# Performance work log

Hardware: AMD Instinct MI355X
Metric: run time of the kernel (lower is better)

Reference implementation:

```python
import jax, jax.numpy as jnp
import numpy as np

NUM_HEADS = 8
D_MODEL = 512
D_Q = D_MODEL // NUM_HEADS
B, S = 4, 2048


def setup_inputs() -> dict:
    key = jax.random.key(0)
    ks = jax.random.split(key, 7)
    bound = 1.0 / np.sqrt(D_MODEL)  # kaiming_uniform with a=sqrt(5) on fan_in=d_model
    return {
        "x_query": jax.random.normal(ks[0], (B, S, D_MODEL), dtype=jnp.float32),
        "x_key": jax.random.normal(ks[1], (B, S, D_MODEL), dtype=jnp.float32),
        "x_value": jax.random.normal(ks[2], (B, S, D_MODEL), dtype=jnp.float32),
        "Q": jax.random.uniform(ks[3], (NUM_HEADS, D_MODEL, D_Q), minval=-bound, maxval=bound, dtype=jnp.float32),
        "K": jax.random.uniform(ks[4], (NUM_HEADS, D_MODEL, D_Q), minval=-bound, maxval=bound, dtype=jnp.float32),
        "V": jax.random.uniform(ks[5], (NUM_HEADS, D_MODEL, D_Q), minval=-bound, maxval=bound, dtype=jnp.float32),
        "Wout": jax.random.uniform(ks[6], (D_MODEL, D_MODEL), minval=-bound, maxval=bound, dtype=jnp.float32),
    }


def reference(x_query, x_key, x_value, Q, K, V, Wout):
    # per-head projections: [B,S,d_model] x [H,d_model,d_q] -> [B,H,S,d_q]
    q = jnp.einsum('bsd,hdq->bhsq', x_query, Q)
    k = jnp.einsum('bsd,hdq->bhsq', x_key, K)
    v = jnp.einsum('bsd,hdq->bhsq', x_value, V)
    scale = 1.0 / jnp.sqrt(jnp.asarray(q.shape[-1], q.dtype))
    scores = jnp.einsum('bhsq,bhtq->bhst', q, k) * scale  # [B,H,S,S]
    attn = jax.nn.softmax(scores, axis=-1)
    heads = jnp.einsum('bhst,bhtq->bhsq', attn, v)  # [B,H,S,d_q]
    # faithful to original: .view(B, S, -1) on [B,H,S,d_q] layout (no transpose)
    concat = heads.reshape(heads.shape[0], heads.shape[2], -1)
    return concat @ Wout.T
```

## Files before the change

kernel.cpp:

```cpp
#include <hip/hip_runtime.h>
#include <math.h>

#define BATCH 4
#define SEQ   2048
#define DM    512
#define NH    8
#define DQ    64
#define BS    (BATCH*SEQ)
#define APAD  72

#define QSCALE 0.18033688011112042f

typedef short  short8   __attribute__((ext_vector_type(8)));
typedef float  floatx4  __attribute__((ext_vector_type(4)));
typedef float  floatx16 __attribute__((ext_vector_type(16)));
typedef unsigned short ushort8 __attribute__((ext_vector_type(8)));
typedef unsigned uintx2 __attribute__((ext_vector_type(2)));
typedef unsigned uintx4 __attribute__((ext_vector_type(4)));

__device__ __forceinline__ unsigned short f2bf(float f) {
    return (unsigned short)((__float_as_uint(f) + 0x8000u) >> 16);
}
__device__ __forceinline__ unsigned pack2bf(float a, float b) {
    unsigned ua = __float_as_uint(a) + 0x8000u;
    unsigned ub = __float_as_uint(b) + 0x8000u;
    return __builtin_amdgcn_perm(ub, ua, 0x07060302u);
}

__global__ __launch_bounds__(256) void convert_w_kernel(
    const float* __restrict__ Wq, const float* __restrict__ Wk,
    const float* __restrict__ Wv, const float* __restrict__ Wo,
    unsigned short* __restrict__ wt, unsigned short* __restrict__ wo)
{
    const int which = blockIdx.y;
    const int idx = blockIdx.x * 256 + threadIdx.x;
    if (which == 3) {
        float4 v = *(const float4*)(Wo + (size_t)idx * 4);
        uint2 o;
        o.x = pack2bf(v.x, v.y);
        o.y = pack2bf(v.z, v.w);
        *(uint2*)(wo + (size_t)idx * 4) = o;
    } else {
        const float* W = (which == 0) ? Wq : (which == 1) ? Wk : Wv;
        const int n   = idx >> 7;
        const int dd0 = (idx & 127) * 4;
        const int h = n >> 6, d = n & 63;
        uint2 o;
        o.x = pack2bf(W[((size_t)h * DM + dd0 + 0) * DQ + d],
                      W[((size_t)h * DM + dd0 + 1) * DQ + d]);
        o.y = pack2bf(W[((size_t)h * DM + dd0 + 2) * DQ + d],
                      W[((size_t)h * DM + dd0 + 3) * DQ + d]);
        *(uint2*)(wt + (size_t)which * (DM * DM) + (size_t)n * DM + dd0) = o;
    }
}

__global__ __launch_bounds__(256) void qkv_gemm_kernel(
    const float* __restrict__ Xq, const float* __restrict__ Xk,
    const float* __restrict__ Xv, const unsigned short* __restrict__ wt,
    unsigned short* __restrict__ Oq, unsigned short* __restrict__ Ok,
    unsigned short* __restrict__ Ovt)
{
    __shared__ unsigned short As[128][APAD];
    __shared__ unsigned short Bs[128][APAD];

    const int which = blockIdx.z;
    const float* X = (which == 0) ? Xq : (which == 1) ? Xk : Xv;
    const unsigned short* Bt = wt + (size_t)which * (DM * DM);

    const int m0 = blockIdx.x * 128;
    const int n0 = blockIdx.y * 128;
    const int t = threadIdx.x, w = t >> 6, lane = t & 63;
    const int quad = lane >> 4, qr = lane & 15;
    const int arow = t >> 4;
    const int acol = (t & 15) * 4;
    const int brow = t >> 3;
    const int bcol = (t & 7) * 8;
    const int mw = 64 * (w >> 1), nw = 64 * (w & 1);

    floatx4 acc[4][4] = {};
    float4  areg[8];
    ushort8 breg[4];

    #pragma unroll
    for (int i = 0; i < 8; ++i)
        areg[i] = *(const float4*)(X + (size_t)(m0 + i * 16 + arow) * DM + acol);
    #pragma unroll
    for (int i = 0; i < 4; ++i)
        breg[i] = *(const ushort8*)(Bt + (size_t)(n0 + i * 32 + brow) * DM + bcol);

    for (int k0 = 0; k0 < DM; k0 += 64) {
        __syncthreads();
        #pragma unroll
        for (int i = 0; i < 8; ++i) {
            uint2 o;
            o.x = pack2bf(areg[i].x, areg[i].y);
            o.y = pack2bf(areg[i].z, areg[i].w);
            *(uint2*)&As[i * 16 + arow][acol] = o;
        }
        #pragma unroll
        for (int i = 0; i < 4; ++i)
            *(ushort8*)&Bs[i * 32 + brow][bcol] = breg[i];
        __syncthreads();

        if (k0 + 64 < DM) {
            #pragma unroll
            for (int i = 0; i < 8; ++i)
                areg[i] = *(const float4*)(X + (size_t)(m0 + i * 16 + arow) * DM + k0 + 64 + acol);
            #pragma unroll
            for (int i = 0; i < 4; ++i)
                breg[i] = *(const ushort8*)(Bt + (size_t)(n0 + i * 32 + brow) * DM + k0 + 64 + bcol);
        }

        #pragma unroll
        for (int kh = 0; kh < 2; ++kh) {
            short8 af[4], bf[4];
            #pragma unroll
            for (int si = 0; si < 4; ++si)
                af[si] = *(const short8*)&As[mw + 16 * si + qr][kh * 32 + quad * 8];
            #pragma unroll
            for (int sj = 0; sj < 4; ++sj)
                bf[sj] = *(const short8*)&Bs[nw + 16 * sj + qr][kh * 32 + quad * 8];
            #pragma unroll
            for (int si = 0; si < 4; ++si)
                #pragma unroll
                for (int sj = 0; sj < 4; ++sj)
                    acc[si][sj] = __builtin_amdgcn_mfma_f32_16x16x32_bf16(
                        af[si], bf[sj], acc[si][sj], 0, 0, 0);
        }
    }

    const float osc = (which == 0) ? QSCALE : 1.0f;
    if (which < 2) {
        unsigned short* O = (which == 0) ? Oq : Ok;
        #pragma unroll
        for (int si = 0; si < 4; ++si) {
            #pragma unroll
            for (int sj = 0; sj < 4; ++sj) {
                const int col = n0 + nw + 16 * sj + qr;
                const int h = col >> 6, d = col & 63;
                #pragma unroll
                for (int r = 0; r < 4; ++r) {
                    const int row = m0 + mw + 16 * si + quad * 4 + r;
                    const int b = row >> 11, s = row & (SEQ - 1);
                    O[((size_t)(b * NH + h) * SEQ + s) * DQ + d] = f2bf(acc[si][sj][r] * osc);
                }
            }
        }
    } else {
        #pragma unroll
        for (int si = 0; si < 4; ++si) {
            #pragma unroll
            for (int sj = 0; sj < 4; ++sj) {
                const int col = n0 + nw + 16 * sj + qr;
                const int h = col >> 6, d = col & 63;
                #pragma unroll
                for (int r = 0; r < 4; ++r) {
                    const int row = m0 + mw + 16 * si + quad * 4 + r;
                    const int b = row >> 11, s = row & (SEQ - 1);
                    Ovt[((size_t)(b * NH + h) * DQ + d) * SEQ + s] = f2bf(acc[si][sj][r]);
                }
            }
        }
    }
}

__global__ __launch_bounds__(256) void out_gemm_kernel(
    const unsigned short* __restrict__ A, const unsigned short* __restrict__ Bt,
    float* __restrict__ C)
{
    __shared__ unsigned short As[64][APAD];
    __shared__ unsigned short Bs[128][APAD];

    const int m0 = blockIdx.x * 64;
    const int n0 = blockIdx.y * 128;
    const int t = threadIdx.x, w = t >> 6, lane = t & 63;
    const int quad = lane >> 4, qr = lane & 15;
    const int brow = t >> 3;
    const int bcol = (t & 7) * 8;
    const int mw = 32 * (w >> 1), nw = 64 * (w & 1);

    floatx4 acc[2][4] = {};
    ushort8 areg[2], breg[4];

    #pragma unroll
    for (int i = 0; i < 2; ++i)
        areg[i] = *(const ushort8*)(A + (size_t)(m0 + i * 32 + brow) * DM + bcol);
    #pragma unroll
    for (int i = 0; i < 4; ++i)
        breg[i] = *(const ushort8*)(Bt + (size_t)(n0 + i * 32 + brow) * DM + bcol);

    for (int k0 = 0; k0 < DM; k0 += 64) {
        __syncthreads();
        #pragma unroll
        for (int i = 0; i < 2; ++i)
            *(ushort8*)&As[i * 32 + brow][bcol] = areg[i];
        #pragma unroll
        for (int i = 0; i < 4; ++i)
            *(ushort8*)&Bs[i * 32 + brow][bcol] = breg[i];
        __syncthreads();

        if (k0 + 64 < DM) {
            #pragma unroll
            for (int i = 0; i < 2; ++i)
                areg[i] = *(const ushort8*)(A + (size_t)(m0 + i * 32 + brow) * DM + k0 + 64 + bcol);
            #pragma unroll
            for (int i = 0; i < 4; ++i)
                breg[i] = *(const ushort8*)(Bt + (size_t)(n0 + i * 32 + brow) * DM + k0 + 64 + bcol);
        }

        #pragma unroll
        for (int kh = 0; kh < 2; ++kh) {
            short8 af[2], bf[4];
            #pragma unroll
            for (int si = 0; si < 2; ++si)
                af[si] = *(const short8*)&As[mw + 16 * si + qr][kh * 32 + quad * 8];
            #pragma unroll
            for (int sj = 0; sj < 4; ++sj)
                bf[sj] = *(const short8*)&Bs[nw + 16 * sj + qr][kh * 32 + quad * 8];
            #pragma unroll
            for (int si = 0; si < 2; ++si)
                #pragma unroll
                for (int sj = 0; sj < 4; ++sj)
                    acc[si][sj] = __builtin_amdgcn_mfma_f32_16x16x32_bf16(
                        af[si], bf[sj], acc[si][sj], 0, 0, 0);
        }
    }

    #pragma unroll
    for (int si = 0; si < 2; ++si) {
        #pragma unroll
        for (int sj = 0; sj < 4; ++sj) {
            const int col = n0 + nw + 16 * sj + qr;
            #pragma unroll
            for (int r = 0; r < 4; ++r) {
                const int row = m0 + mw + 16 * si + quad * 4 + r;
                C[(size_t)row * DM + col] = acc[si][sj][r];
            }
        }
    }
}

__global__ __launch_bounds__(256, 4) void attn_kernel(
    const unsigned short* __restrict__ Qp, const unsigned short* __restrict__ Kp,
    const unsigned short* __restrict__ Vtp, unsigned short* __restrict__ Hd)
{
    __shared__ unsigned short smem[3 * 64 * 64];
    unsigned short (*Qs)[64]  = (unsigned short (*)[64])(smem);
    unsigned short (*Ks)[64]  = (unsigned short (*)[64])(smem + 64 * 64);
    unsigned short (*Vts)[64] = (unsigned short (*)[64])(smem + 2 * 64 * 64);

    const int f    = blockIdx.x;
    const int xcd  = f & 7;
    const int slot = f >> 3;
    const int tile = slot & 31;
    const int bhi  = (slot >> 5) * 8 + xcd;
    const int b = bhi >> 3, h = bhi & 7;

    const int s0 = tile * 64;
    const size_t bh    = (size_t)(b * NH + h);
    const size_t base  = bh * SEQ * DQ;
    const size_t vbase = bh * DQ * SEQ;

    const int t    = threadIdx.x;
    const int w    = t >> 6;
    const int lane = t & 63;
    const int qh   = w >> 1;
    const int kh   = w & 1;
    const int ln31 = lane & 31;
    const int lh   = lane >> 5;

    {
        const unsigned short* g = Qp + base + (size_t)s0 * DQ;
        #pragma unroll
        for (int i = 0; i < 2; ++i) {
            const int c = t + 256 * i;
            const int row = c >> 3, col8 = (c & 7) * 8;
            *(ushort8*)&Qs[row][col8 ^ ((row & 7) * 8)] = *(const ushort8*)(g + row * DQ + col8);
        }
    }
    __syncthreads();
    short8 bq[4];
    {
        const int qrow = 32 * qh + ln31;
        #pragma unroll
        for (int s = 0; s < 4; ++s)
            bq[s] = *(const short8*)&Qs[qrow][(16 * s + lh * 8) ^ ((qrow & 7) * 8)];
    }

    floatx16 accO[2] = {};
    float l_lane = 0.f;

    ushort8 kreg[2], vreg[2];
    {
        const unsigned short* gk = Kp + base;
        const unsigned short* gv = Vtp + vbase;
        #pragma unroll
        for (int i = 0; i < 2; ++i) {
            const int c = t + 256 * i;
            const int row = c >> 3, col8 = (c & 7) * 8;
            kreg[i] = *(const ushort8*)(gk + row * DQ + col8);
            vreg[i] = *(const ushort8*)(gv + (size_t)row * SEQ + col8);
        }
    }

    for (int kt = 0; kt < SEQ; kt += 64) {
        __syncthreads();
        #pragma unroll
        for (int i = 0; i < 2; ++i) {
            const int c = t + 256 * i;
            const int row = c >> 3, col8 = (c & 7) * 8;
            const int sc = col8 ^ ((row & 7) * 8);
            *(ushort8*)&Ks[row][sc]  = kreg[i];
            *(ushort8*)&Vts[row][sc] = vreg[i];
        }
        __syncthreads();

        if (kt + 64 < SEQ) {
            const unsigned short* gk = Kp + base + (size_t)(kt + 64) * DQ;
            const unsigned short* gv = Vtp + vbase + (kt + 64);
            #pragma unroll
            for (int i = 0; i < 2; ++i) {
                const int c = t + 256 * i;
                const int row = c >> 3, col8 = (c & 7) * 8;
                kreg[i] = *(const ushort8*)(gk + row * DQ + col8);
                vreg[i] = *(const ushort8*)(gv + (size_t)row * SEQ + col8);
            }
        }

        floatx16 z = {};
        __builtin_amdgcn_s_setprio(1);
        {
            const int krow = 32 * kh + ln31;
            #pragma unroll
            for (int s = 0; s < 4; ++s) {
                const short8 ak = *(const short8*)&Ks[krow][(16 * s + lh * 8) ^ ((krow & 7) * 8)];
                z = __builtin_amdgcn_mfma_f32_32x32x16_bf16(ak, bq[s], z, 0, 0, 0);
            }
        }
        __builtin_amdgcn_s_setprio(0);

        unsigned wg[4][2];
        #pragma unroll
        for (int g = 0; g < 4; ++g) {
            const float p0 = __builtin_amdgcn_exp2f(z[4 * g + 0]);
            const float p1 = __builtin_amdgcn_exp2f(z[4 * g + 1]);
            const float p2 = __builtin_amdgcn_exp2f(z[4 * g + 2]);
            const float p3 = __builtin_amdgcn_exp2f(z[4 * g + 3]);
            l_lane += (p0 + p1) + (p2 + p3);
            wg[g][0] = pack2bf(p0, p1);
            wg[g][1] = pack2bf(p2, p3);
        }

        const uintx2 e0 = __builtin_amdgcn_permlane32_swap(wg[0][0], wg[1][0], false, false);
        const uintx2 e1 = __builtin_amdgcn_permlane32_swap(wg[0][1], wg[1][1], false, false);
        const uintx2 e2 = __builtin_amdgcn_permlane32_swap(wg[2][0], wg[3][0], false, false);
        const uintx2 e3 = __builtin_amdgcn_permlane32_swap(wg[2][1], wg[3][1], false, false);
        uintx4 ua0, ua1;
        ua0[0] = e0[0]; ua0[1] = e1[0]; ua0[2] = e0[1]; ua0[3] = e1[1];
        ua1[0] = e2[0]; ua1[1] = e3[0]; ua1[2] = e2[1]; ua1[3] = e3[1];
        const short8 ap0 = __builtin_bit_cast(short8, ua0);
        const short8 ap1 = __builtin_bit_cast(short8, ua1);

        __builtin_amdgcn_s_setprio(1);
        #pragma unroll
        for (int a = 0; a < 2; ++a) {
            const int vrow = 32 * a + ln31;
            #pragma unroll
            for (int s = 0; s < 2; ++s) {
                const short8 bv = *(const short8*)&Vts[vrow][(32 * kh + 16 * s + lh * 8) ^ ((vrow & 7) * 8)];
                accO[a] = __builtin_amdgcn_mfma_f32_32x32x16_bf16(
                    (s == 0) ? ap0 : ap1, bv, accO[a], 0, 0, 0);
            }
        }
        __builtin_amdgcn_s_setprio(0);
    }

    float l2 = l_lane + __shfl_xor(l_lane, 32);
    float* Obuf = (float*)smem;
    float* lbuf = (float*)(smem + 3 * 64 * 64 - 256);
    __syncthreads();

    if (kh == 0) {
        if (lane < 32) lbuf[qh * 32 + lane] = l2;
        #pragma unroll
        for (int a = 0; a < 2; ++a)
            #pragma unroll
            for (int r = 0; r < 16; ++r) {
                const int qrow = (r & 3) + 8 * (r >> 2) + 4 * lh;
                Obuf[(32 * qh + qrow) * 66 + 32 * a + ln31] = accO[a][r];
            }
    }
    __syncthreads();

    if (kh == 1) {
        const float ltot = l2 + lbuf[qh * 32 + ln31];
        if (lane < 32) lbuf[64 + qh * 32 + lane] = 1.0f / ltot;
        #pragma unroll
        for (int a = 0; a < 2; ++a)
            #pragma unroll
            for (int r = 0; r < 16; ++r) {
                const int qrow = (r & 3) + 8 * (r >> 2) + 4 * lh;
                const float o = accO[a][r] + Obuf[(32 * qh + qrow) * 66 + 32 * a + ln31];
                const float iv = lbuf[64 + qh * 32 + qrow];
                Hd[base + (size_t)(s0 + 32 * qh + qrow) * DQ + 32 * a + ln31] = f2bf(o * iv);
            }
    }
}

extern "C" void kernel_launch(void* const* d_in, const int* in_sizes, int n_in,
                              void* d_out, int out_size, void* d_ws, size_t ws_size,
                              hipStream_t stream) {
    const float* xq = (const float*)d_in[0];
    const float* xk = (const float*)d_in[1];
    const float* xv = (const float*)d_in[2];
    const float* Qw = (const float*)d_in[3];
    const float* Kw = (const float*)d_in[4];
    const float* Vw = (const float*)d_in[5];
    const float* Wo = (const float*)d_in[6];
    float* out = (float*)d_out;

    unsigned short* ws = (unsigned short*)d_ws;
    unsigned short* wt    = ws;
    unsigned short* wo    = ws + (size_t)786432;
    unsigned short* q_ws  = ws + (size_t)1048576;
    unsigned short* k_ws  = ws + (size_t)5242880;
    unsigned short* vt_ws = ws + (size_t)9437184;
    unsigned short* h_ws  = ws + (size_t)13631488;

    convert_w_kernel<<<dim3(256, 4), 256, 0, stream>>>(Qw, Kw, Vw, Wo, wt, wo);
    qkv_gemm_kernel<<<dim3(64, 4, 3), 256, 0, stream>>>(xq, xk, xv, wt, q_ws, k_ws, vt_ws);
    attn_kernel<<<dim3(1024), 256, 0, stream>>>(q_ws, k_ws, vt_ws, h_ws);
    out_gemm_kernel<<<dim3(128, 4), 256, 0, stream>>>(h_ws, wo, out);
}
```

Measured before the change: 185.6 us.

## Load K/V MFMA operands directly from global into registers, drop LDS staging

The V projection now writes V^T in a blocked layout of 64x64 tiles, so each key tile is contiguous. The attention kernel drops LDS staging for Q, K and V and loads MFMA operands straight from global memory into registers, prefetching the next tile after each MFMA group. This removes the two __syncthreads per iteration and the LDS traffic. In exchange, each wave re-reads K/V from global or L2 (redundant across waves), and global load latency is exposed with only single-step register prefetch.

After: 255.0 us. 37.4% more time.

```diff
diff --git a/kernel.cpp b/kernel.cpp
--- a/kernel.cpp
+++ b/kernel.cpp
@@ -157,7 +157,8 @@
                 for (int r = 0; r < 4; ++r) {
                     const int row = m0 + mw + 16 * si + quad * 4 + r;
                     const int b = row >> 11, s = row & (SEQ - 1);
-                    Ovt[((size_t)(b * NH + h) * DQ + d) * SEQ + s] = f2bf(acc[si][sj][r]);
+                    Ovt[(size_t)(b * NH + h) * (DQ * SEQ)
+                        + ((size_t)((s >> 6) * 64 + d) << 6) + (s & 63)] = f2bf(acc[si][sj][r]);
                 }
             }
         }
@@ -242,12 +243,9 @@
 
 __global__ __launch_bounds__(256, 4) void attn_kernel(
     const unsigned short* __restrict__ Qp, const unsigned short* __restrict__ Kp,
-    const unsigned short* __restrict__ Vtp, unsigned short* __restrict__ Hd)
+    const unsigned short* __restrict__ Vbp, unsigned short* __restrict__ Hd)
 {
-    __shared__ unsigned short smem[3 * 64 * 64];
-    unsigned short (*Qs)[64]  = (unsigned short (*)[64])(smem);
-    unsigned short (*Ks)[64]  = (unsigned short (*)[64])(smem + 64 * 64);
-    unsigned short (*Vts)[64] = (unsigned short (*)[64])(smem + 2 * 64 * 64);
+    __shared__ float epi[64 * 66 + 128];
 
     const int f    = blockIdx.x;
     const int xcd  = f & 7;
@@ -269,75 +267,45 @@
     const int ln31 = lane & 31;
     const int lh   = lane >> 5;
 
-    {
-        const unsigned short* g = Qp + base + (size_t)s0 * DQ;
-        #pragma unroll
-        for (int i = 0; i < 2; ++i) {
-            const int c = t + 256 * i;
-            const int row = c >> 3, col8 = (c & 7) * 8;
-            *(ushort8*)&Qs[row][col8 ^ ((row & 7) * 8)] = *(const ushort8*)(g + row * DQ + col8);
-        }
-    }
-    __syncthreads();
     short8 bq[4];
     {
-        const int qrow = 32 * qh + ln31;
+        const unsigned short* gq = Qp + base + (size_t)(s0 + 32 * qh + ln31) * DQ + lh * 8;
         #pragma unroll
         for (int s = 0; s < 4; ++s)
-            bq[s] = *(const short8*)&Qs[qrow][(16 * s + lh * 8) ^ ((qrow & 7) * 8)];
-    }
+            bq[s] = *(const short8*)(gq + 16 * s);
+    }
+
+    const unsigned short* pK = Kp + base + (size_t)(32 * kh + ln31) * DQ + lh * 8;
+    const unsigned short* pV = Vbp + vbase + (size_t)ln31 * 64 + 32 * kh + lh * 8;
 
     floatx16 accO[2] = {};
     float l_lane = 0.f;
 
-    ushort8 kreg[2], vreg[2];
-    {
-        const unsigned short* gk = Kp + base;
-        const unsigned short* gv = Vtp + vbase;
-        #pragma unroll
-        for (int i = 0; i < 2; ++i) {
-            const int c = t + 256 * i;
-            const int row = c >> 3, col8 = (c & 7) * 8;
-            kreg[i] = *(const ushort8*)(gk + row * DQ + col8);
-            vreg[i] = *(const ushort8*)(gv + (size_t)row * SEQ + col8);
-        }
-    }
+    short8 ak[4], bv[4];
+    #pragma unroll
+    for (int s = 0; s < 4; ++s)
+        ak[s] = *(const short8*)(pK + 16 * s);
+    #pragma unroll
+    for (int a = 0; a < 2; ++a)
+        #pragma unroll
+        for (int s = 0; s < 2; ++s)
+            bv[a * 2 + s] = *(const short8*)(pV + a * 2048 + 16 * s);
 
     for (int kt = 0; kt < SEQ; kt += 64) {
-        __syncthreads();
-        #pragma unroll
-        for (int i = 0; i < 2; ++i) {
-            const int c = t + 256 * i;
-            const int row = c >> 3, col8 = (c & 7) * 8;
-            const int sc = col8 ^ ((row & 7) * 8);
-            *(ushort8*)&Ks[row][sc]  = kreg[i];
-            *(ushort8*)&Vts[row][sc] = vreg[i];
-        }
-        __syncthreads();
-
-        if (kt + 64 < SEQ) {
-            const unsigned short* gk = Kp + base + (size_t)(kt + 64) * DQ;
-            const unsigned short* gv = Vtp + vbase + (kt + 64);
-            #pragma unroll
-            for (int i = 0; i < 2; ++i) {
-                const int c = t + 256 * i;
-                const int row = c >> 3, col8 = (c & 7) * 8;
-                kreg[i] = *(const ushort8*)(gk + row * DQ + col8);
-                vreg[i] = *(const ushort8*)(gv + (size_t)row * SEQ + col8);
-            }
-        }
-
         floatx16 z = {};
         __builtin_amdgcn_s_setprio(1);
+        #pragma unroll
+        for (int s = 0; s < 4; ++s)
+            z = __builtin_amdgcn_mfma_f32_32x32x16_bf16(ak[s], bq[s], z, 0, 0, 0);
+        __builtin_amdgcn_s_setprio(0);
+
+        const int ktn = (kt + 64 < SEQ) ? kt + 64 : kt;
         {
-            const int krow = 32 * kh + ln31;
-            #pragma unroll
-            for (int s = 0; s < 4; ++s) {
-                const short8 ak = *(const short8*)&Ks[krow][(16 * s + lh * 8) ^ ((krow & 7) * 8)];
-                z = __builtin_amdgcn_mfma_f32_32x32x16_bf16(ak, bq[s], z, 0, 0, 0);
-            }
-        }
-        __builtin_amdgcn_s_setprio(0);
+            const unsigned short* nK = pK + (size_t)ktn * DQ;
+            #pragma unroll
+            for (int s = 0; s < 4; ++s)
+                ak[s] = *(const short8*)(nK + 16 * s);
+        }
 
         unsigned wg[4][2];
         #pragma unroll
@@ -364,21 +332,24 @@
         __builtin_amdgcn_s_setprio(1);
         #pragma unroll
         for (int a = 0; a < 2; ++a) {
-            const int vrow = 32 * a + ln31;
-            #pragma unroll
-            for (int s = 0; s < 2; ++s) {
-                const short8 bv = *(const short8*)&Vts[vrow][(32 * kh + 16 * s + lh * 8) ^ ((vrow & 7) * 8)];
-                accO[a] = __builtin_amdgcn_mfma_f32_32x32x16_bf16(
-                    (s == 0) ? ap0 : ap1, bv, accO[a], 0, 0, 0);
-            }
+            accO[a] = __builtin_amdgcn_mfma_f32_32x32x16_bf16(ap0, bv[a * 2 + 0], accO[a], 0, 0, 0);
+            accO[a] = __builtin_amdgcn_mfma_f32_32x32x16_bf16(ap1, bv[a * 2 + 1], accO[a], 0, 0, 0);
         }
         __builtin_amdgcn_s_setprio(0);
+
+        {
+            const unsigned short* nV = pV + (size_t)(ktn >> 6) * 4096;
+            #pragma unroll
+            for (int a = 0; a < 2; ++a)
+                #pragma unroll
+                for (int s = 0; s < 2; ++s)
+                    bv[a * 2 + s] = *(const short8*)(nV + a * 2048 + 16 * s);
+        }
     }
 
     float l2 = l_lane + __shfl_xor(l_lane, 32);
-    float* Obuf = (float*)smem;
-    float* lbuf = (float*)(smem + 3 * 64 * 64 - 256);
-    __syncthreads();
+    float* Obuf = epi;
+    float* lbuf = epi + 64 * 66;
 
     if (kh == 0) {
         if (lane < 32) lbuf[qh * 32 + lane] = l2;
```
